# Kernel optimization log

Hardware: AMD Instinct MI355X
Metric: run time of the kernel (lower is better)

## Reference

```python
import jax, jax.numpy as jnp
import numpy as np


def _fo_pool(f, z):
    # c_t = f_t * c_{t-1} + z_t, c_0 = 0, scanned over axis 1 (seq).
    # Associative combine: (a1,b1) * (a2,b2) = (a1*a2, a2*b1 + b2)
    def combine(left, right):
        a1, b1 = left
        a2, b2 = right
        return a1 * a2, a2 * b1 + b2
    _, c = jax.lax.associative_scan(combine, (f, z), axis=1)
    return c


def setup_inputs() -> dict:
    key = jax.random.key(0)
    ks = jax.random.split(key, 10)
    B, S, D_in, D_model, D_mlp, n_cls = 32, 2048, 512, 1024, 1024, 128
    s = 0.02
    return {
        "x":  jax.random.normal(ks[0], (B, S, D_in), dtype=jnp.float32),
        "W":  jax.random.normal(ks[1], (D_in, 3 * D_model), dtype=jnp.float32) * s,  # Linear, bias=False
        "V":  jax.random.normal(ks[2], (D_in, 3 * D_model), dtype=jnp.float32) * s,
        "Vb": jax.random.normal(ks[3], (3 * D_model,), dtype=jnp.float32) * s,
        "W0": jax.random.normal(ks[4], (D_model, D_mlp), dtype=jnp.float32) * s,
        "b0": jax.random.normal(ks[5], (D_mlp,), dtype=jnp.float32) * s,
        "W1": jax.random.normal(ks[6], (D_mlp, D_mlp), dtype=jnp.float32) * s,
        "b1": jax.random.normal(ks[7], (D_mlp,), dtype=jnp.float32) * s,
        "W2": jax.random.normal(ks[8], (D_mlp, n_cls), dtype=jnp.float32) * s,
        "b2": jax.random.normal(ks[9], (n_cls,), dtype=jnp.float32) * s,
    }


def reference(x, W, V, Vb, W0, b0, W1, b1, W2, b2):
    # kernel_size=2 pre: W(x) + V(x shifted right by one, zero-padded)
    xprev = jnp.pad(x[:, :-1, :], ((0, 0), (1, 0), (0, 0)))  # [B,S,D_in]
    pre = jnp.einsum('bsd,dk->bsk', x, W) + jnp.einsum('bsd,dk->bsk', xprev, V) + Vb
    f, z, o = jnp.split(pre, 3, axis=-1)
    f = jax.nn.sigmoid(f)
    z = (1.0 - f) * jnp.tanh(z)
    o = jax.nn.sigmoid(o)
    c = _fo_pool(f, z)          # [B,S,D_model]
    h = c * o
    q = h[:, -1, :]             # last timestep
    # dropout is identity at inference (training=False)
    q = jax.nn.relu(q @ W0 + b0)
    q = jax.nn.relu(q @ W1 + b1)
    return q @ W2 + b2
```

## Files before the change

kernel.cpp:

```cpp
#include <hip/hip_runtime.h>
#include <cstdint>
#include <cstddef>


typedef __attribute__((ext_vector_type(8))) short short8;
typedef __attribute__((ext_vector_type(4))) float f32x4;

#define ZERO_OFF_E 6291456u
#define XB_OFF_E   8388608u
#define U_LDS_BASE 8256

__device__ __forceinline__ unsigned short f2bf(float f) {
  unsigned int u = __float_as_uint(f);
  u += 0x7fffu + ((u >> 16) & 1u);
  return (unsigned short)(u >> 16);
}

__device__ __forceinline__ unsigned stage_addr(int r, int c) {
  return (unsigned)(r * 64 + (((c + r + (r >> 2)) & 3) << 4));
}

__device__ __forceinline__ float sigmoidf_fast(float x) {
  return 1.f / (1.f + __expf(-x));
}
__device__ __forceinline__ float tanhf_fast(float x) {
  float a = fabsf(x);
  float e = __expf(-2.f * a);
  float t = (1.f - e) / (1.f + e);
  return copysignf(t, x);
}

__device__ __forceinline__ void gload_lds16(const void* g, const char* lds) {
  __builtin_amdgcn_global_load_lds(
      (const __attribute__((address_space(1))) void*)(uintptr_t)g,
      (__attribute__((address_space(3))) void*)(uint32_t)(uintptr_t)lds, 16, 0, 0);
}

__global__ void prologue_kernel(const float* __restrict__ x, const float* __restrict__ W,
                                const float* __restrict__ V,
                                const float* __restrict__ b0, const float* __restrict__ b1,
                                const float* __restrict__ b2,
                                unsigned short* __restrict__ xb, unsigned short* __restrict__ U,
                                float* __restrict__ q0, float* __restrict__ q1,
                                float* __restrict__ out, uint4* __restrict__ zpg) {
  __shared__ float T[64 * 65];
  const int bx = blockIdx.x;
  if (bx < 8192) {
    int base = bx * 1024 + threadIdx.x;
#pragma unroll
    for (int i = 0; i < 4; ++i) {
      int gid = base + i * 256;
      float4 v = ((const float4*)x)[gid];
      ushort4 o;
      o.x = f2bf(v.x); o.y = f2bf(v.y); o.z = f2bf(v.z); o.w = f2bf(v.w);
      ((ushort4*)xb)[gid] = o;
    }
  } else if (bx < 8704) {
    const int u = bx - 8192;
    const int j0 = (u & 31) * 64;
    const int k0 = (u >> 5) * 64;
    const int jl = threadIdx.x & 63;
    const int q  = threadIdx.x >> 6;
    const float* src = (k0 < 512) ? (W + (size_t)k0 * 3072) : (V + (size_t)(k0 - 512) * 3072);
#pragma unroll 4
    for (int i = 0; i < 16; ++i) {
      int kl = q * 16 + i;
      T[kl * 65 + jl] = src[(size_t)kl * 3072 + j0 + jl];
    }
    __syncthreads();
    const int kl = threadIdx.x & 63;
#pragma unroll 4
    for (int i = 0; i < 16; ++i) {
      int jj = q * 16 + i;
      U[(size_t)(j0 + jj) * 1024 + k0 + kl] = f2bf(T[kl * 65 + jj]);
    }
  } else if (bx < 8832) {
    int gid = (bx - 8704) * 256 + threadIdx.x;
    q0[gid] = b0[gid & 1023];
    q1[gid] = b1[gid & 1023];
    if (gid < 4096) out[gid] = b2[gid & 127];
  } else {
    zpg[threadIdx.x] = make_uint4(0u, 0u, 0u, 0u);
  }
}

__global__ __launch_bounds__(256, 4) void qrnn_main4(
    const unsigned short* __restrict__ wsb, const float* __restrict__ Vb,
    float* __restrict__ Fagg, float* __restrict__ Zagg) {
  __shared__ __align__(16) char smem[36864];

  const int dt = blockIdx.x;
  const int cj = blockIdx.y;
  const int b  = blockIdx.z;

  const int tid = threadIdx.x;
  const int lane = tid & 63;
  const int wid  = tid >> 6;
  const int wm = wid >> 1, wn = wid & 1;
  const int l15 = lane & 15, lc = lane >> 4;
  const int s0 = cj * 128;

  f32x4 acc[4][4];
#pragma unroll
  for (int i = 0; i < 4; ++i)
#pragma unroll
    for (int j = 0; j < 4; ++j) acc[i][j] = f32x4{0.f, 0.f, 0.f, 0.f};

  unsigned eAx[2], eAp[2], eB[2];
#pragma unroll
  for (int i = 0; i < 2; ++i) {
    int row_g = wid * 32 + i * 16 + (lane >> 2);
    int q = (lane & 3) ^ ((row_g >> 1) & 3);
    int tx = s0 + row_g;
    eAx[i] = XB_OFF_E + (unsigned)(b * 2048 + tx) * 512u + (unsigned)(q * 8);
    int tp = s0 - 1 + row_g;
    eAp[i] = (tp < 0) ? (ZERO_OFF_E + (unsigned)(q * 8))
                      : (XB_OFF_E + (unsigned)(b * 2048 + tp) * 512u + (unsigned)(q * 8));
    int jj = (row_g < 64) ? (dt * 64 + row_g) : (1024 + dt * 64 + (row_g - 64));
    eB[i] = (unsigned)jj * 1024u + (unsigned)(q * 8);
  }

  const unsigned swz = (unsigned)((lc ^ ((l15 >> 1) & 3)) << 4);
  const unsigned oA = (unsigned)((wm * 64 + l15) * 64) + swz;
  const unsigned oB = 8192u + (unsigned)((wn * 64 + l15) * 64) + swz;

  auto stage = [&](int kt, int slot) {
    const unsigned sbase = (unsigned)(slot * 16384);
    const bool xp = (kt < 16);
    const unsigned kaddA = xp ? (unsigned)(kt * 32) : (unsigned)((kt - 16) * 32);
    const unsigned kaddB = (unsigned)(kt * 32);
#pragma unroll
    for (int i = 0; i < 2; ++i) {
      unsigned da = (unsigned)__builtin_amdgcn_readfirstlane(
          (int)(sbase + (unsigned)(wid * 2048 + i * 1024)));
      gload_lds16(wsb + ((xp ? eAx[i] : eAp[i]) + kaddA), smem + da);
    }
#pragma unroll
    for (int i = 0; i < 2; ++i) {
      unsigned db = (unsigned)__builtin_amdgcn_readfirstlane(
          (int)(sbase + 8192u + (unsigned)(wid * 2048 + i * 1024)));
      gload_lds16(wsb + (eB[i] + kaddB), smem + db);
    }
  };

  stage(0, 0);

#define KSTEP(KT, SLOT)                                                              \
  {                                                                                  \
    const int kt = (KT);                                                             \
    asm volatile("s_waitcnt vmcnt(0)" ::: "memory");                                 \
    __builtin_amdgcn_s_barrier();                                                    \
    if (kt < 31) stage(kt + 1, (SLOT) ^ 1);                                          \
    const char* buf = smem + (SLOT) * 16384;                                         \
    short8 bfr[4];                                                                   \
    _Pragma("unroll")                                                                \
    for (int nt = 0; nt < 4; ++nt) bfr[nt] = *(const short8*)(buf + oB + nt * 1024); \
    __builtin_amdgcn_s_setprio(1);                                                   \
    _Pragma("unroll")                                                                \
    for (int mt = 0; mt < 4; ++mt) {                                                 \
      short8 afr = *(const short8*)(buf + oA + mt * 1024);                           \
      _Pragma("unroll")                                                              \
      for (int nt = 0; nt < 4; ++nt)                                                 \
        acc[mt][nt] =                                                                \
            __builtin_amdgcn_mfma_f32_16x16x32_bf16(afr, bfr[nt], acc[mt][nt], 0, 0, 0); \
    }                                                                                \
    __builtin_amdgcn_s_setprio(0);                                                   \
  }

#pragma unroll 1
  for (int k2 = 0; k2 < 32; k2 += 2) {
    KSTEP(k2,     0);
    KSTEP(k2 + 1, 1);
  }
#undef KSTEP

  float* fA   = (float*)smem;
  float* tzA  = (float*)(smem + 17408);
  float* segF = (float*)(smem + 34816);
  float* segZ = (float*)(smem + 35840);

  const int d = tid & 63;
  float vb[4];
#pragma unroll
  for (int nt = 0; nt < 4; ++nt)
    vb[nt] = Vb[wn * 1024 + dt * 64 + nt * 16 + l15];

  float F_run = 1.f, Z_run = 0.f;

  for (int ph = 0; ph < 2; ++ph) {
    __syncthreads();
    if (wm == ph) {
      float* dst = (wn == 0) ? fA : tzA;
#pragma unroll
      for (int mt = 0; mt < 4; ++mt)
#pragma unroll
        for (int nt = 0; nt < 4; ++nt)
#pragma unroll
          for (int rg = 0; rg < 4; ++rg) {
            int t = mt * 16 + (lc << 2) + rg;
            int c = nt * 16 + l15;
            float v = acc[mt][nt][rg] + vb[nt];
            v = (wn == 0) ? sigmoidf_fast(v) : tanhf_fast(v);
            dst[t * 68 + c] = v;
          }
    }
    __syncthreads();
    {
      int seg = tid >> 6;
      float F = 1.f, Z = 0.f;
#pragma unroll 4
      for (int i = 0; i < 16; ++i) {
        int t = seg * 16 + i;
        float f  = fA[t * 68 + d];
        float tz = tzA[t * 68 + d];
        float z = (1.f - f) * tz;
        Z = f * Z + z;
        F *= f;
      }
      segF[seg * 64 + d] = F;
      segZ[seg * 64 + d] = Z;
    }
    __syncthreads();
    if (tid < 64) {
#pragma unroll
      for (int sgi = 0; sgi < 4; ++sgi) {
        float Fs = segF[sgi * 64 + tid], Zs = segZ[sgi * 64 + tid];
        Z_run = Fs * Z_run + Zs;
        F_run *= Fs;
      }
    }
  }
  if (tid < 64) {
    size_t o = (((size_t)b * 16 + cj) << 10) + dt * 64 + tid;
    Fagg[o] = F_run;
    Zagg[o] = Z_run;
  }
}

template <bool USE_BF>
__global__ __launch_bounds__(256, 3) void qrnn_main(
    const unsigned short* __restrict__ wsb, const float* __restrict__ xf,
    const float* __restrict__ Vb,
    float* __restrict__ Fagg, float* __restrict__ Zagg) {
  __shared__ __align__(16) char smem[36864];

  const int dt = blockIdx.x;
  const int cj = blockIdx.y;
  const int b  = blockIdx.z;
  const int tid = threadIdx.x;
  const int lane = tid & 63;
  const int wid  = tid >> 6;
  const int wm = wid >> 1, wn = wid & 1;
  const int s0 = cj * 128;
  const int l15 = lane & 15, lc = lane >> 4;

  f32x4 acc[4][4];
#pragma unroll
  for (int i = 0; i < 4; ++i)
#pragma unroll
    for (int j = 0; j < 4; ++j) acc[i][j] = f32x4{0.f, 0.f, 0.f, 0.f};

  unsigned voffA[2];
  size_t offAF[2]; int zAF[2];
#pragma unroll
  for (int p = 0; p < 2; ++p) {
    int cw = tid + p * 256;
    int r = cw >> 2, c = cw & 3;
    int sg = s0 - 1 + r;
    voffA[p] = (sg < 0) ? (ZERO_OFF_E + (unsigned)(c * 8))
                        : (XB_OFF_E + (unsigned)(b * 2048 + sg) * 512u + (unsigned)(c * 8));
    zAF[p] = (sg < 0);
    offAF[p] = ((size_t)(b * 2048 + (sg < 0 ? 0 : sg)) << 9) + c * 8;
  }
  unsigned voffA3 = XB_OFF_E + (unsigned)(b * 2048 + s0 + 127) * 512u + (unsigned)((tid & 3) * 8);
  size_t offAF3 = ((size_t)(b * 2048 + s0 + 127) << 9) + (tid & 3) * 8;

  unsigned voffU[4];
#pragma unroll
  for (int k = 0; k < 4; ++k) {
    int uw = tid + k * 256;
    int r = uw >> 2, c = uw & 3;
    int col = r & 127, half = r >> 7;
    int j = (col < 64) ? (dt * 64 + col) : (1024 + dt * 64 + (col - 64));
    voffU[k] = (unsigned)(j * 1024 + half * 512 + c * 8);
  }

  unsigned wA[2], wU[4];
#pragma unroll
  for (int p = 0; p < 2; ++p) {
    int cw = tid + p * 256;
    wA[p] = stage_addr(cw >> 2, cw & 3);
  }
  const unsigned wA3 = stage_addr(128, tid & 3);
#pragma unroll
  for (int k = 0; k < 4; ++k) {
    int uw = tid + k * 256;
    wU[k] = U_LDS_BASE + stage_addr(uw >> 2, uw & 3);
  }

  unsigned roA[2][4], roU[2][4];
#pragma unroll
  for (int h2 = 0; h2 < 2; ++h2) {
#pragma unroll
    for (int mt = 0; mt < 4; ++mt) {
      int rr = wm * 64 + l15 + mt * 16 + 1 - h2;
      roA[h2][mt] = stage_addr(rr, lc);
    }
#pragma unroll
    for (int nt = 0; nt < 4; ++nt) {
      int rrU = h2 * 128 + wn * 64 + l15 + nt * 16;
      roU[h2][nt] = U_LDS_BASE + stage_addr(rrU, lc);
    }
  }

  uint4 pA0, pA1, pA3, pU0, pU1, pU2, pU3;

  auto load_stage = [&](int s) {
    const unsigned short* cur = wsb + s * 32;
    if constexpr (USE_BF) {
      pA0 = *(const uint4*)(cur + voffA[0]);
      pA1 = *(const uint4*)(cur + voffA[1]);
      if (tid < 4) pA3 = *(const uint4*)(cur + voffA3);
    } else {
      const float* curf = xf + s * 32;
#pragma unroll
      for (int p = 0; p < 2; ++p) {
        uint4 v = make_uint4(0u, 0u, 0u, 0u);
        if (!zAF[p]) {
          float4 a0 = *(const float4*)(curf + offAF[p]);
          float4 a1 = *(const float4*)(curf + offAF[p] + 4);
          v.x = (unsigned)f2bf(a0.x) | ((unsigned)f2bf(a0.y) << 16);
          v.y = (unsigned)f2bf(a0.z) | ((unsigned)f2bf(a0.w) << 16);
          v.z = (unsigned)f2bf(a1.x) | ((unsigned)f2bf(a1.y) << 16);
          v.w = (unsigned)f2bf(a1.z) | ((unsigned)f2bf(a1.w) << 16);
        }
        if (p == 0) pA0 = v; else pA1 = v;
      }
      if (tid < 4) {
        float4 a0 = *(const float4*)(curf + offAF3);
        float4 a1 = *(const float4*)(curf + offAF3 + 4);
        pA3.x = (unsigned)f2bf(a0.x) | ((unsigned)f2bf(a0.y) << 16);
        pA3.y = (unsigned)f2bf(a0.z) | ((unsigned)f2bf(a0.w) << 16);
        pA3.z = (unsigned)f2bf(a1.x) | ((unsigned)f2bf(a1.y) << 16);
        pA3.w = (unsigned)f2bf(a1.z) | ((unsigned)f2bf(a1.w) << 16);
      }
    }
    pU0 = *(const uint4*)(cur + voffU[0]);
    pU1 = *(const uint4*)(cur + voffU[1]);
    pU2 = *(const uint4*)(cur + voffU[2]);
    pU3 = *(const uint4*)(cur + voffU[3]);
  };

  load_stage(0);

#pragma unroll 1
  for (int s = 0; s < 16; ++s) {
    __syncthreads();
    *(uint4*)(smem + wA[0]) = pA0;
    *(uint4*)(smem + wA[1]) = pA1;
    if (tid < 4) *(uint4*)(smem + wA3) = pA3;
    *(uint4*)(smem + wU[0]) = pU0;
    *(uint4*)(smem + wU[1]) = pU1;
    *(uint4*)(smem + wU[2]) = pU2;
    *(uint4*)(smem + wU[3]) = pU3;
    __syncthreads();
    if (s < 15) load_stage(s + 1);
#pragma unroll
    for (int h2 = 0; h2 < 2; ++h2) {
      short8 bfr[4];
#pragma unroll
      for (int nt = 0; nt < 4; ++nt)
        bfr[nt] = *(const short8*)(smem + roU[h2][nt]);
#pragma unroll
      for (int mt = 0; mt < 4; ++mt) {
        short8 afr = *(const short8*)(smem + roA[h2][mt]);
#pragma unroll
        for (int nt = 0; nt < 4; ++nt)
          acc[mt][nt] = __builtin_amdgcn_mfma_f32_16x16x32_bf16(afr, bfr[nt], acc[mt][nt], 0, 0, 0);
      }
    }
  }

  float* fA   = (float*)smem;
  float* tzA  = (float*)(smem + 17408);
  float* segF = (float*)(smem + 34816);
  float* segZ = (float*)(smem + 35840);

  const int d = tid & 63;
  float vb[4];
#pragma unroll
  for (int nt = 0; nt < 4; ++nt)
    vb[nt] = Vb[wn * 1024 + dt * 64 + nt * 16 + l15];

  float F_run = 1.f, Z_run = 0.f;

  for (int ph = 0; ph < 2; ++ph) {
    __syncthreads();
    if (wm == ph) {
      float* dst = (wn == 0) ? fA : tzA;
#pragma unroll
      for (int mt = 0; mt < 4; ++mt)
#pragma unroll
        for (int nt = 0; nt < 4; ++nt)
#pragma unroll
          for (int rg = 0; rg < 4; ++rg) {
            int t = mt * 16 + ((lane >> 4) << 2) + rg;
            int c = nt * 16 + l15;
            float v = acc[mt][nt][rg] + vb[nt];
            v = (wn == 0) ? sigmoidf_fast(v) : tanhf_fast(v);
            dst[t * 68 + c] = v;
          }
    }
    __syncthreads();
    {
      int seg = tid >> 6;
      float F = 1.f, Z = 0.f;
#pragma unroll 4
      for (int i = 0; i < 16; ++i) {
        int t = seg * 16 + i;
        float f  = fA[t * 68 + d];
        float tz = tzA[t * 68 + d];
        float z = (1.f - f) * tz;
        Z = f * Z + z;
        F *= f;
      }
      segF[seg * 64 + d] = F;
      segZ[seg * 64 + d] = Z;
    }
    __syncthreads();
    if (tid < 64) {
#pragma unroll
      for (int sgi = 0; sgi < 4; ++sgi) {
        float Fs = segF[sgi * 64 + tid], Zs = segZ[sgi * 64 + tid];
        Z_run = Fs * Z_run + Zs;
        F_run *= Fs;
      }
    }
  }
  if (tid < 64) {
    size_t o = (((size_t)b * 16 + cj) << 10) + dt * 64 + tid;
    Fagg[o] = F_run;
    Zagg[o] = Z_run;
  }
}

__global__ void head_kernel(const float* __restrict__ x, const float* __restrict__ W,
                            const float* __restrict__ V, const float* __restrict__ Vb,
                            const float* __restrict__ Fagg, const float* __restrict__ Zagg,
                            float* __restrict__ h, int nch) {
  __shared__ float red[4][64];
  const int dl = threadIdx.x & 63;
  const int w  = threadIdx.x >> 6;
  const int d = blockIdx.x * 64 + dl;
  const int b = blockIdx.y;

  const float* xl = x + ((size_t)b * 2048 + 2047) * 512;
  const float* xp = xl - 512;
  const float* Wc = W + 2048 + d;
  const float* Vc = V + 2048 + d;
  float po = 0.f;
  const int k0 = w * 128;
#pragma unroll 8
  for (int k = k0; k < k0 + 128; ++k) {
    po += xl[k] * Wc[(size_t)k * 3072];
    po += xp[k] * Vc[(size_t)k * 3072];
  }
  red[w][dl] = po;
  __syncthreads();
  if (w == 0) {
    po = red[0][dl] + red[1][dl] + red[2][dl] + red[3][dl] + Vb[2048 + d];
    float c = 0.f;
    for (int j = 0; j < nch; ++j) {
      size_t o = (((size_t)b * nch + j) << 10) + d;
      c = Fagg[o] * c + Zagg[o];
    }
    h[((size_t)b << 10) + d] = c * sigmoidf_fast(po);
  }
}

__global__ void mlp_atomic_kernel(const float* __restrict__ in, const float* __restrict__ Wt,
                                  float* __restrict__ out, int K, int N, int relu_in) {
  __shared__ float red[4][64];
  const int nl = threadIdx.x & 63;
  const int w  = threadIdx.x >> 6;
  const int n = blockIdx.x * 64 + nl;
  const int b = blockIdx.y;
  const int k0 = blockIdx.z * (K >> 2) + w * (K >> 4);
  const float* row = in + (size_t)b * K;
  const float* Wc = Wt + n;
  float s = 0.f;
#pragma unroll 8
  for (int k = k0; k < k0 + (K >> 4); ++k) {
    float v = row[k];
    if (relu_in) v = fmaxf(v, 0.f);
    s += v * Wc[(size_t)k * N];
  }
  red[w][nl] = s;
  __syncthreads();
  if (w == 0) {
    s = red[0][nl] + red[1][nl] + red[2][nl] + red[3][nl];
    atomicAdd(&out[(size_t)b * N + n], s);
  }
}

extern "C" void kernel_launch(void* const* d_in, const int* in_sizes, int n_in,
                              void* d_out, int out_size, void* d_ws, size_t ws_size,
                              hipStream_t stream) {
  const float* x  = (const float*)d_in[0];
  const float* W  = (const float*)d_in[1];
  const float* V  = (const float*)d_in[2];
  const float* Vb = (const float*)d_in[3];
  const float* W0 = (const float*)d_in[4];
  const float* b0 = (const float*)d_in[5];
  const float* W1 = (const float*)d_in[6];
  const float* b1 = (const float*)d_in[7];
  const float* W2 = (const float*)d_in[8];
  const float* b2 = (const float*)d_in[9];

  char* ws = (char*)d_ws;
  unsigned short* U = (unsigned short*)(ws);
  float* Fagg = (float*)(ws + (size_t)4 * 1024 * 1024);
  float* Zagg = (float*)(ws + (size_t)6 * 1024 * 1024);
  float* h    = (float*)(ws + (size_t)8 * 1024 * 1024);
  float* q0   = (float*)(ws + (size_t)8 * 1024 * 1024 + 256 * 1024);
  float* q1   = (float*)(ws + (size_t)8 * 1024 * 1024 + 512 * 1024);
  uint4* zpg  = (uint4*)(ws + (size_t)12 * 1024 * 1024);
  unsigned short* xb = (unsigned short*)(ws + (size_t)16 * 1024 * 1024);

  const size_t need_bf = (size_t)16 * 1024 * 1024 + (size_t)67108864;
  int use_bf = (ws_size >= need_bf) ? 1 : 0;

  prologue_kernel<<<8833, 256, 0, stream>>>(x, W, V, b0, b1, b2, xb, U, q0, q1,
                                            (float*)d_out, zpg);
  if (use_bf) {
    qrnn_main4<<<dim3(16, 16, 32), 256, 0, stream>>>((const unsigned short*)ws, Vb, Fagg, Zagg);
  } else {
    qrnn_main<false><<<dim3(16, 16, 32), 256, 0, stream>>>((const unsigned short*)ws, x,
                                                           Vb, Fagg, Zagg);
  }
  head_kernel<<<dim3(16, 32), 256, 0, stream>>>(x, W, V, Vb, Fagg, Zagg, h, 16);
  mlp_atomic_kernel<<<dim3(16, 32, 4), 256, 0, stream>>>(h, W0, q0, 1024, 1024, 0);
  mlp_atomic_kernel<<<dim3(16, 32, 4), 256, 0, stream>>>(q0, W1, q1, 1024, 1024, 1);
  mlp_atomic_kernel<<<dim3(2, 32, 4), 256, 0, stream>>>(q1, W2, (float*)d_out, 1024, 128, 1);
}
```

Measured before the change: 617.9 us.

## Reuse shared x tile for both shift halves in main QRNN GEMM

The main projection GEMM stops loading separate x and x-shifted A tiles over 32 k-steps. Each of 16 stages now loads one 129-row x window plus both W and V slices of U, and the current and previous-timestep operands come from row-offset LDS reads. This cuts global-to-LDS traffic for the activation operand and halves the number of barrier-synchronised stages. In exchange the LDS footprint grows to about 48 KB, and launch bounds drop from 4 to 3 blocks per CU, which lowers occupancy.

```diff
diff --git a/kernel.cpp b/kernel.cpp
--- a/kernel.cpp
+++ b/kernel.cpp
@@ -8,7 +8,8 @@
 
 #define ZERO_OFF_E 6291456u
 #define XB_OFF_E   8388608u
-#define U_LDS_BASE 8256
+#define SLOT_STRIDE 24640
+#define U_BASE 8256
 
 __device__ __forceinline__ unsigned short f2bf(float f) {
   unsigned int u = __float_as_uint(f);
@@ -84,21 +85,20 @@
   }
 }
 
-__global__ __launch_bounds__(256, 4) void qrnn_main4(
+__global__ __launch_bounds__(256, 3) void qrnn_hyb(
     const unsigned short* __restrict__ wsb, const float* __restrict__ Vb,
     float* __restrict__ Fagg, float* __restrict__ Zagg) {
-  __shared__ __align__(16) char smem[36864];
+  __shared__ __align__(16) char smem[2 * SLOT_STRIDE];
 
   const int dt = blockIdx.x;
   const int cj = blockIdx.y;
   const int b  = blockIdx.z;
-
   const int tid = threadIdx.x;
   const int lane = tid & 63;
   const int wid  = tid >> 6;
   const int wm = wid >> 1, wn = wid & 1;
+  const int s0 = cj * 128;
   const int l15 = lane & 15, lc = lane >> 4;
-  const int s0 = cj * 128;
 
   f32x4 acc[4][4];
 #pragma unroll
@@ -106,73 +106,96 @@
 #pragma unroll
     for (int j = 0; j < 4; ++j) acc[i][j] = f32x4{0.f, 0.f, 0.f, 0.f};
 
-  unsigned eAx[2], eAp[2], eB[2];
+  unsigned vA[2], vA2, vU[4];
 #pragma unroll
   for (int i = 0; i < 2; ++i) {
-    int row_g = wid * 32 + i * 16 + (lane >> 2);
-    int q = (lane & 3) ^ ((row_g >> 1) & 3);
-    int tx = s0 + row_g;
-    eAx[i] = XB_OFF_E + (unsigned)(b * 2048 + tx) * 512u + (unsigned)(q * 8);
-    int tp = s0 - 1 + row_g;
-    eAp[i] = (tp < 0) ? (ZERO_OFF_E + (unsigned)(q * 8))
-                      : (XB_OFF_E + (unsigned)(b * 2048 + tp) * 512u + (unsigned)(q * 8));
-    int jj = (row_g < 64) ? (dt * 64 + row_g) : (1024 + dt * 64 + (row_g - 64));
-    eB[i] = (unsigned)jj * 1024u + (unsigned)(q * 8);
-  }
-
-  const unsigned swz = (unsigned)((lc ^ ((l15 >> 1) & 3)) << 4);
-  const unsigned oA = (unsigned)((wm * 64 + l15) * 64) + swz;
-  const unsigned oB = 8192u + (unsigned)((wn * 64 + l15) * 64) + swz;
-
-  auto stage = [&](int kt, int slot) {
-    const unsigned sbase = (unsigned)(slot * 16384);
-    const bool xp = (kt < 16);
-    const unsigned kaddA = xp ? (unsigned)(kt * 32) : (unsigned)((kt - 16) * 32);
-    const unsigned kaddB = (unsigned)(kt * 32);
+    int pc = wid * 128 + i * 64 + lane;
+    int r = pc >> 2;
+    int q = ((pc & 3) - r - (r >> 2)) & 3;
+    int sg = s0 - 1 + r;
+    vA[i] = (sg < 0) ? (ZERO_OFF_E + (unsigned)(q * 8))
+                     : (XB_OFF_E + (unsigned)(b * 2048 + sg) * 512u + (unsigned)(q * 8));
+  }
+  vA2 = XB_OFF_E + (unsigned)(b * 2048 + s0 + 127) * 512u + (unsigned)((lane & 3) * 8);
+#pragma unroll
+  for (int k = 0; k < 4; ++k) {
+    int pc = wid * 256 + k * 64 + lane;
+    int r = pc >> 2;
+    int col = r & 127, half = r >> 7;
+    int j = (col < 64) ? (dt * 64 + col) : (1024 + dt * 64 + (col - 64));
+    int q = ((pc & 3) - r - (r >> 2)) & 3;
+    vU[k] = (unsigned)(j * 1024 + half * 512 + q * 8);
+  }
+
+  unsigned roA[2][4], roU[2][4];
+#pragma unroll
+  for (int h2 = 0; h2 < 2; ++h2) {
+#pragma unroll
+    for (int mt = 0; mt < 4; ++mt) {
+      int rr = wm * 64 + l15 + mt * 16 + 1 - h2;
+      roA[h2][mt] = stage_addr(rr, lc);
+    }
+#pragma unroll
+    for (int nt = 0; nt < 4; ++nt) {
+      int rrU = h2 * 128 + wn * 64 + l15 + nt * 16;
+      roU[h2][nt] = U_BASE + stage_addr(rrU, lc);
+    }
+  }
+
+  auto stage = [&](int s, int slot) {
+    const unsigned short* cur = wsb + s * 32;
+    const unsigned sb = (unsigned)(slot * SLOT_STRIDE);
 #pragma unroll
     for (int i = 0; i < 2; ++i) {
-      unsigned da = (unsigned)__builtin_amdgcn_readfirstlane(
-          (int)(sbase + (unsigned)(wid * 2048 + i * 1024)));
-      gload_lds16(wsb + ((xp ? eAx[i] : eAp[i]) + kaddA), smem + da);
-    }
-#pragma unroll
-    for (int i = 0; i < 2; ++i) {
-      unsigned db = (unsigned)__builtin_amdgcn_readfirstlane(
-          (int)(sbase + 8192u + (unsigned)(wid * 2048 + i * 1024)));
-      gload_lds16(wsb + (eB[i] + kaddB), smem + db);
+      unsigned d = (unsigned)__builtin_amdgcn_readfirstlane(
+          (int)(sb + (unsigned)((wid * 128 + i * 64) * 16)));
+      gload_lds16(cur + vA[i], smem + d);
+    }
+    {
+      unsigned d2 = (unsigned)__builtin_amdgcn_readfirstlane((int)(sb + 8192u));
+      if (lane < 4) gload_lds16(cur + vA2, smem + d2);
+    }
+#pragma unroll
+    for (int k = 0; k < 4; ++k) {
+      unsigned d = (unsigned)__builtin_amdgcn_readfirstlane(
+          (int)(sb + (unsigned)(U_BASE + (wid * 256 + k * 64) * 16)));
+      gload_lds16(cur + vU[k], smem + d);
     }
   };
 
   stage(0, 0);
 
-#define KSTEP(KT, SLOT)                                                              \
-  {                                                                                  \
-    const int kt = (KT);                                                             \
-    asm volatile("s_waitcnt vmcnt(0)" ::: "memory");                                 \
-    __builtin_amdgcn_s_barrier();                                                    \
-    if (kt < 31) stage(kt + 1, (SLOT) ^ 1);                                          \
-    const char* buf = smem + (SLOT) * 16384;                                         \
-    short8 bfr[4];                                                                   \
-    _Pragma("unroll")                                                                \
-    for (int nt = 0; nt < 4; ++nt) bfr[nt] = *(const short8*)(buf + oB + nt * 1024); \
-    __builtin_amdgcn_s_setprio(1);                                                   \
-    _Pragma("unroll")                                                                \
-    for (int mt = 0; mt < 4; ++mt) {                                                 \
-      short8 afr = *(const short8*)(buf + oA + mt * 1024);                           \
-      _Pragma("unroll")                                                              \
-      for (int nt = 0; nt < 4; ++nt)                                                 \
-        acc[mt][nt] =                                                                \
-            __builtin_amdgcn_mfma_f32_16x16x32_bf16(afr, bfr[nt], acc[mt][nt], 0, 0, 0); \
-    }                                                                                \
-    __builtin_amdgcn_s_setprio(0);                                                   \
+#define SSTEP(S, SLOT, LAST)                                                           \
+  {                                                                                    \
+    asm volatile("s_waitcnt vmcnt(0)" ::: "memory");                                   \
+    __builtin_amdgcn_s_barrier();                                                      \
+    if (!(LAST)) stage((S) + 1, (SLOT) ^ 1);                                           \
+    const char* buf = smem + (SLOT) * SLOT_STRIDE;                                     \
+    _Pragma("unroll")                                                                  \
+    for (int h2 = 0; h2 < 2; ++h2) {                                                   \
+      short8 bfr[4];                                                                   \
+      _Pragma("unroll")                                                                \
+      for (int nt = 0; nt < 4; ++nt)                                                   \
+        bfr[nt] = *(const short8*)(buf + roU[h2][nt]);                                 \
+      __builtin_amdgcn_s_setprio(1);                                                   \
+      _Pragma("unroll")                                                                \
+      for (int mt = 0; mt < 4; ++mt) {                                                 \
+        short8 afr = *(const short8*)(buf + roA[h2][mt]);                              \
+        _Pragma("unroll")                                                              \
+        for (int nt = 0; nt < 4; ++nt)                                                 \
+          acc[mt][nt] = __builtin_amdgcn_mfma_f32_16x16x32_bf16(afr, bfr[nt],          \
+                                                                acc[mt][nt], 0, 0, 0); \
+      }                                                                                \
+      __builtin_amdgcn_s_setprio(0);                                                   \
+    }                                                                                  \
   }
 
 #pragma unroll 1
-  for (int k2 = 0; k2 < 32; k2 += 2) {
-    KSTEP(k2,     0);
-    KSTEP(k2 + 1, 1);
-  }
-#undef KSTEP
+  for (int s2 = 0; s2 < 16; s2 += 2) {
+    SSTEP(s2,     0, false);
+    SSTEP(s2 + 1, 1, (s2 + 1) == 15);
+  }
+#undef SSTEP
 
   float* fA   = (float*)smem;
   float* tzA  = (float*)(smem + 17408);
@@ -295,7 +318,7 @@
 #pragma unroll
   for (int k = 0; k < 4; ++k) {
     int uw = tid + k * 256;
-    wU[k] = U_LDS_BASE + stage_addr(uw >> 2, uw & 3);
+    wU[k] = U_BASE + stage_addr(uw >> 2, uw & 3);
   }
 
   unsigned roA[2][4], roU[2][4];
@@ -309,7 +332,7 @@
 #pragma unroll
     for (int nt = 0; nt < 4; ++nt) {
       int rrU = h2 * 128 + wn * 64 + l15 + nt * 16;
-      roU[h2][nt] = U_LDS_BASE + stage_addr(rrU, lc);
+      roU[h2][nt] = U_BASE + stage_addr(rrU, lc);
     }
   }
 
@@ -533,7 +556,7 @@
   prologue_kernel<<<8833, 256, 0, stream>>>(x, W, V, b0, b1, b2, xb, U, q0, q1,
                                             (float*)d_out, zpg);
   if (use_bf) {
-    qrnn_main4<<<dim3(16, 16, 32), 256, 0, stream>>>((const unsigned short*)ws, Vb, Fagg, Zagg);
+    qrnn_hyb<<<dim3(16, 16, 32), 256, 0, stream>>>((const unsigned short*)ws, Vb, Fagg, Zagg);
   } else {
     qrnn_main<false><<<dim3(16, 16, 32), 256, 0, stream>>>((const unsigned short*)ws, x,
                                                            Vb, Fagg, Zagg);
```

Result: no change. 628.1 us (+1.6%).
